# Performance work log

Hardware: AMD Instinct MI355X
Metric: run time of the kernel (lower is better)

Reference implementation:

```python
import jax, jax.numpy as jnp
import numpy as np

B, C, D, H, W = 8, 512, 512, 128, 128


def setup_inputs() -> dict:
    key = jax.random.key(0)
    ks = jax.random.split(key, 6)
    s = 0.02  # small init scale for stable softmax
    return {
        "x": jax.random.normal(ks[0], (B, C, H, W), dtype=jnp.float32),
        "context": jax.random.normal(ks[1], (B, D), dtype=jnp.float32),
        "Wq": jax.random.normal(ks[2], (C, D), dtype=jnp.float32) * s,
        "bq": jnp.ones((C,), dtype=jnp.float32),
        "Wk": jax.random.normal(ks[3], (C, C), dtype=jnp.float32) * s,
        "bk": jnp.zeros((C,), dtype=jnp.float32),
        "Wv": jax.random.normal(ks[4], (C, C), dtype=jnp.float32) * s,
        "bv": jnp.zeros((C,), dtype=jnp.float32),
    }


def reference(x, context, Wq, bq, Wk, bk, Wv, bv):
    # x: (B,C,H,W), context: (B,D)
    scale = x.shape[1] ** (-0.5)
    # q_proj: Linear(D -> C), single query per batch element
    q = context @ Wq.T + bq                      # (B, C)
    # 1x1 convs are channel-mixing GEMMs over the spatial grid
    k = jnp.einsum('bchw,oc->bohw', x, Wk) + bk[None, :, None, None]  # (B,C,H,W)
    v = jnp.einsum('bchw,oc->bohw', x, Wv) + bv[None, :, None, None]  # (B,C,H,W)
    # attention logits over the HW positions (query length == 1)
    logits = jnp.einsum('bc,bchw->bhw', q, k) * scale                 # (B,H,W)
    Bn, Hn, Wn = logits.shape
    attn = jax.nn.softmax(logits.reshape(Bn, Hn * Wn), axis=-1).reshape(Bn, Hn, Wn)
    # attention-pooled value -> channel gate
    gate = jnp.einsum('bhw,bchw->bc', attn, v)                        # (B,C)
    return x * gate[:, :, None, None]
```

## Files before the change

### kernel.cpp

```cpp
#include <hip/hip_runtime.h>
#include <math.h>

#define BB   8
#define CC   512
#define DD   512
#define HW   16384
#define HW4  4096
#define NCHUNK 64


__global__ __launch_bounds__(256) void k_qk2(const float* __restrict__ ctx,
                                             const float* __restrict__ Wq,
                                             const float* __restrict__ bq,
                                             const float* __restrict__ Wk,
                                             float* __restrict__ qk) {
    __shared__ float qs[CC];
    int b    = blockIdx.x >> 1;
    int half = blockIdx.x & 1;
    const float4* cr = (const float4*)(ctx + (size_t)b * DD);
    for (int c = threadIdx.x; c < CC; c += 256) {
        const float4* wr = (const float4*)(Wq + (size_t)c * DD);
        float acc = 0.f;
        #pragma unroll 8
        for (int d = 0; d < DD / 4; ++d) {
            float4 a = cr[d], w = wr[d];
            acc += a.x * w.x + a.y * w.y + a.z * w.z + a.w * w.w;
        }
        qs[c] = acc + bq[c];
    }
    __syncthreads();
    int c = half * 256 + threadIdx.x;
    float acc = 0.f;
    #pragma unroll 8
    for (int o = 0; o < CC; ++o) acc += qs[o] * Wk[(size_t)o * CC + c];
    qk[b * CC + c] = acc;
}

__global__ __launch_bounds__(256) void k_logits_p(const float* __restrict__ x,
                                                  const float* __restrict__ qk,
                                                  float* __restrict__ p,
                                                  float* __restrict__ stats) {
    __shared__ float  qs[CC];
    __shared__ float4 comb[3][64];
    int b     = blockIdx.x >> 6;
    int chunk = blockIdx.x & 63;
    int wave = threadIdx.x >> 6, lane = threadIdx.x & 63;
    int hw4 = chunk * 64 + lane;
    for (int i = threadIdx.x; i < CC; i += 256) qs[i] = qk[b * CC + i];
    __syncthreads();
    const float4* x4 = (const float4*)x;
    size_t base = (size_t)b * CC * HW4 + (size_t)(wave * 128) * HW4 + hw4;
    float ax = 0.f, ay = 0.f, az = 0.f, aw = 0.f;
    #pragma unroll 8
    for (int c = 0; c < 128; ++c) {
        float4 v = x4[base + (size_t)c * HW4];
        float w = qs[wave * 128 + c];
        ax += w * v.x; ay += w * v.y; az += w * v.z; aw += w * v.w;
    }
    if (wave > 0) {
        float4 pp = { ax, ay, az, aw };
        comb[wave - 1][lane] = pp;
    }
    __syncthreads();
    if (wave == 0) {
        #pragma unroll
        for (int w2 = 0; w2 < 3; ++w2) {
            float4 pp = comb[w2][lane];
            ax += pp.x; ay += pp.y; az += pp.z; aw += pp.w;
        }
        const float scale = 0.04419417382415922f;
        ax *= scale; ay *= scale; az *= scale; aw *= scale;
        float m = fmaxf(fmaxf(ax, ay), fmaxf(az, aw));
        #pragma unroll
        for (int off = 32; off; off >>= 1) m = fmaxf(m, __shfl_xor(m, off));
        float4 o;
        o.x = expf(ax - m); o.y = expf(ay - m);
        o.z = expf(az - m); o.w = expf(aw - m);
        float s = o.x + o.y + o.z + o.w;
        #pragma unroll
        for (int off = 32; off; off >>= 1) s += __shfl_xor(s, off);
        ((float4*)p)[(size_t)b * HW4 + hw4] = o;
        if (lane == 0) { stats[blockIdx.x * 2] = m; stats[blockIdx.x * 2 + 1] = s; }
    }
}

__global__ __launch_bounds__(256) void k_pool(const float* __restrict__ x,
                                              const float* __restrict__ p,
                                              const float* __restrict__ stats,
                                              float* __restrict__ pooled) {
    __shared__ float wgt[NCHUNK];
    int bc = blockIdx.x;
    int b  = bc >> 9;
    int tid = threadIdx.x;
    if (tid < 64) {
        float mc = stats[(b * NCHUNK + tid) * 2];
        float sc = stats[(b * NCHUNK + tid) * 2 + 1];
        float m = mc;
        #pragma unroll
        for (int off = 32; off; off >>= 1) m = fmaxf(m, __shfl_xor(m, off));
        float w = expf(mc - m);
        float d = w * sc;
        #pragma unroll
        for (int off = 32; off; off >>= 1) d += __shfl_xor(d, off);
        wgt[tid] = w / d;
    }
    __syncthreads();
    const float4* xr = (const float4*)x + (size_t)bc * HW4;
    const float4* pr = (const float4*)p + (size_t)b  * HW4;
    float acc = 0.f;
    #pragma unroll 8
    for (int i = tid; i < HW4; i += 256) {
        float4 xv = xr[i], pv = pr[i];
        acc += wgt[i >> 6] * (xv.x * pv.x + xv.y * pv.y + xv.z * pv.z + xv.w * pv.w);
    }
    for (int off = 32; off; off >>= 1) acc += __shfl_down(acc, off);
    __shared__ float red[4];
    if ((tid & 63) == 0) red[tid >> 6] = acc;
    __syncthreads();
    if (tid == 0) pooled[bc] = red[0] + red[1] + red[2] + red[3];
}

__global__ __launch_bounds__(256) void k_gate(const float* __restrict__ pooled,
                                              const float* __restrict__ Wv,
                                              const float* __restrict__ bv,
                                              float* __restrict__ gate) {
    int t = blockIdx.x * 256 + threadIdx.x;
    int b = t >> 9, o = t & (CC - 1);
    const float4* pr = (const float4*)(pooled + (size_t)b * CC);
    const float4* wr = (const float4*)(Wv + (size_t)o * CC);
    float acc = 0.f;
    #pragma unroll 8
    for (int i = 0; i < CC / 4; ++i) {
        float4 pv = pr[i], w = wr[i];
        acc += pv.x * w.x + pv.y * w.y + pv.z * w.z + pv.w * w.w;
    }
    gate[t] = acc + bv[o];
}

__global__ __launch_bounds__(256) void k_out(const float* __restrict__ x,
                                             const float* __restrict__ gate,
                                             float* __restrict__ out) {
    int bc = blockIdx.x;
    float g = gate[bc];
    const float4* xr = (const float4*)x   + (size_t)bc * HW4;
    float4*       orow = (float4*)out     + (size_t)bc * HW4;
    #pragma unroll 8
    for (int i = threadIdx.x; i < HW4; i += 256) {
        float4 v = xr[i];
        float4 o = { v.x * g, v.y * g, v.z * g, v.w * g };
        orow[i] = o;
    }
}

extern "C" void kernel_launch(void* const* d_in, const int* in_sizes, int n_in,
                              void* d_out, int out_size, void* d_ws, size_t ws_size,
                              hipStream_t stream) {
    const float* x   = (const float*)d_in[0];
    const float* ctx = (const float*)d_in[1];
    const float* Wq  = (const float*)d_in[2];
    const float* bq  = (const float*)d_in[3];
    const float* Wk  = (const float*)d_in[4];
    const float* Wv  = (const float*)d_in[6];
    const float* bv  = (const float*)d_in[7];
    float* out = (float*)d_out;

    float* ws     = (float*)d_ws;
    float* qk     = ws;
    float* pooled = ws + 4096;
    float* gate   = ws + 8192;
    float* stats  = ws + 12288;
    float* p      = ws + 13312;

    k_qk2     <<<  16, 256, 0, stream>>>(ctx, Wq, bq, Wk, qk);
    k_logits_p<<< 512, 256, 0, stream>>>(x, qk, p, stats);
    k_pool    <<<4096, 256, 0, stream>>>(x, p, stats, pooled);
    k_gate    <<<  16, 256, 0, stream>>>(pooled, Wv, bv, gate);
    k_out     <<<4096, 256, 0, stream>>>(x, gate, out);
}
```

Before: 618.9 us.

## Fuse logits, softmax and pooling into one pass over x with partial sums

Merges the logits/softmax kernel and the pooling kernel so each block loads a tile of x (all channels, 32 positions) into registers once. From those registers it computes the logits, a local softmax and per-channel weighted partial sums. A new combine kernel rescales the 512 per-chunk partials with online-softmax statistics to produce the pooled vector. This removes one full read of x and the p round-trip, at the cost of writing and reading 8×512×512 partials and using more registers per thread.

```diff
diff --git a/kernel.cpp b/kernel.cpp
--- a/kernel.cpp
+++ b/kernel.cpp
@@ -6,7 +6,7 @@
 #define DD   512
 #define HW   16384
 #define HW4  4096
-#define NCHUNK 64
+#define NCH  512
 
 
 __global__ __launch_bounds__(256) void k_qk2(const float* __restrict__ ctx,
@@ -36,88 +36,105 @@
     qk[b * CC + c] = acc;
 }
 
-__global__ __launch_bounds__(256) void k_logits_p(const float* __restrict__ x,
+__global__ __launch_bounds__(512, 4) void k_fused(const float* __restrict__ x,
                                                   const float* __restrict__ qk,
-                                                  float* __restrict__ p,
+                                                  float* __restrict__ part,
                                                   float* __restrict__ stats) {
-    __shared__ float  qs[CC];
-    __shared__ float4 comb[3][64];
-    int b     = blockIdx.x >> 6;
-    int chunk = blockIdx.x & 63;
-    int wave = threadIdx.x >> 6, lane = threadIdx.x & 63;
-    int hw4 = chunk * 64 + lane;
-    for (int i = threadIdx.x; i < CC; i += 256) qs[i] = qk[b * CC + i];
+    __shared__ float qs[CC];
+    __shared__ float4 comb[7][8];
+    __shared__ float4 p4s[8];
+    __shared__ __align__(16) float partLDS[CC];
+    int b   = blockIdx.x >> 9;
+    int cid = blockIdx.x & (NCH - 1);
+    int tid = threadIdx.x;
+    int w = tid >> 6, l = tid & 63;
+    int lg = l >> 3, lp = l & 7;
+    for (int i = tid; i < CC; i += 512) qs[i] = qk[b * CC + i];
     __syncthreads();
     const float4* x4 = (const float4*)x;
-    size_t base = (size_t)b * CC * HW4 + (size_t)(wave * 128) * HW4 + hw4;
-    float ax = 0.f, ay = 0.f, az = 0.f, aw = 0.f;
-    #pragma unroll 8
-    for (int c = 0; c < 128; ++c) {
-        float4 v = x4[base + (size_t)c * HW4];
-        float w = qs[wave * 128 + c];
-        ax += w * v.x; ay += w * v.y; az += w * v.z; aw += w * v.w;
+    size_t base = ((size_t)(b * CC + 64 * w + lg)) * HW4 + cid * 8 + lp;
+    float4 xr[8];
+    #pragma unroll
+    for (int it = 0; it < 8; ++it) xr[it] = x4[base + (size_t)it * 8 * HW4];
+    float4 la = { 0.f, 0.f, 0.f, 0.f };
+    #pragma unroll
+    for (int it = 0; it < 8; ++it) {
+        float qv = qs[64 * w + 8 * it + lg];
+        la.x += qv * xr[it].x; la.y += qv * xr[it].y;
+        la.z += qv * xr[it].z; la.w += qv * xr[it].w;
     }
-    if (wave > 0) {
-        float4 pp = { ax, ay, az, aw };
-        comb[wave - 1][lane] = pp;
+    #pragma unroll
+    for (int st = 8; st <= 32; st <<= 1) {
+        la.x += __shfl_xor(la.x, st); la.y += __shfl_xor(la.y, st);
+        la.z += __shfl_xor(la.z, st); la.w += __shfl_xor(la.w, st);
+    }
+    if (w > 0 && l < 8) comb[w - 1][l] = la;
+    __syncthreads();
+    if (w == 0 && l < 8) {
+        #pragma unroll
+        for (int i = 0; i < 7; ++i) {
+            float4 t = comb[i][l];
+            la.x += t.x; la.y += t.y; la.z += t.z; la.w += t.w;
+        }
+        const float scale = 0.04419417382415922f;
+        la.x *= scale; la.y *= scale; la.z *= scale; la.w *= scale;
+        float m = fmaxf(fmaxf(la.x, la.y), fmaxf(la.z, la.w));
+        m = fmaxf(m, __shfl_xor(m, 1));
+        m = fmaxf(m, __shfl_xor(m, 2));
+        m = fmaxf(m, __shfl_xor(m, 4));
+        float4 p;
+        p.x = expf(la.x - m); p.y = expf(la.y - m);
+        p.z = expf(la.z - m); p.w = expf(la.w - m);
+        float s = p.x + p.y + p.z + p.w;
+        s += __shfl_xor(s, 1); s += __shfl_xor(s, 2); s += __shfl_xor(s, 4);
+        p4s[l] = p;
+        if (l == 0) { stats[blockIdx.x * 2] = m; stats[blockIdx.x * 2 + 1] = s; }
     }
     __syncthreads();
-    if (wave == 0) {
-        #pragma unroll
-        for (int w2 = 0; w2 < 3; ++w2) {
-            float4 pp = comb[w2][lane];
-            ax += pp.x; ay += pp.y; az += pp.z; aw += pp.w;
-        }
-        const float scale = 0.04419417382415922f;
-        ax *= scale; ay *= scale; az *= scale; aw *= scale;
-        float m = fmaxf(fmaxf(ax, ay), fmaxf(az, aw));
-        #pragma unroll
-        for (int off = 32; off; off >>= 1) m = fmaxf(m, __shfl_xor(m, off));
-        float4 o;
-        o.x = expf(ax - m); o.y = expf(ay - m);
-        o.z = expf(az - m); o.w = expf(aw - m);
-        float s = o.x + o.y + o.z + o.w;
-        #pragma unroll
-        for (int off = 32; off; off >>= 1) s += __shfl_xor(s, off);
-        ((float4*)p)[(size_t)b * HW4 + hw4] = o;
-        if (lane == 0) { stats[blockIdx.x * 2] = m; stats[blockIdx.x * 2 + 1] = s; }
+    float4 pw = p4s[lp];
+    #pragma unroll
+    for (int it = 0; it < 8; ++it) {
+        float r = pw.x * xr[it].x + pw.y * xr[it].y + pw.z * xr[it].z + pw.w * xr[it].w;
+        r += __shfl_xor(r, 1); r += __shfl_xor(r, 2); r += __shfl_xor(r, 4);
+        if (lp == 0) partLDS[64 * w + 8 * it + lg] = r;
     }
+    __syncthreads();
+    if (tid < CC / 4)
+        ((float4*)(part + (size_t)blockIdx.x * CC))[tid] = ((float4*)partLDS)[tid];
 }
 
-__global__ __launch_bounds__(256) void k_pool(const float* __restrict__ x,
-                                              const float* __restrict__ p,
-                                              const float* __restrict__ stats,
-                                              float* __restrict__ pooled) {
-    __shared__ float wgt[NCHUNK];
-    int bc = blockIdx.x;
-    int b  = bc >> 9;
+__global__ __launch_bounds__(256) void k_combine(const float* __restrict__ part,
+                                                 const float* __restrict__ stats,
+                                                 float* __restrict__ pooled) {
+    __shared__ float wgt[NCH];
+    __shared__ float redm[4], reds[4];
+    int b = blockIdx.x >> 1, half = blockIdx.x & 1;
     int tid = threadIdx.x;
-    if (tid < 64) {
-        float mc = stats[(b * NCHUNK + tid) * 2];
-        float sc = stats[(b * NCHUNK + tid) * 2 + 1];
-        float m = mc;
-        #pragma unroll
-        for (int off = 32; off; off >>= 1) m = fmaxf(m, __shfl_xor(m, off));
-        float w = expf(mc - m);
-        float d = w * sc;
-        #pragma unroll
-        for (int off = 32; off; off >>= 1) d += __shfl_xor(d, off);
-        wgt[tid] = w / d;
-    }
+    float m1 = stats[((size_t)b * NCH + tid) * 2];
+    float s1 = stats[((size_t)b * NCH + tid) * 2 + 1];
+    float m2 = stats[((size_t)b * NCH + tid + 256) * 2];
+    float s2 = stats[((size_t)b * NCH + tid + 256) * 2 + 1];
+    float m = fmaxf(m1, m2);
+    #pragma unroll
+    for (int off = 32; off; off >>= 1) m = fmaxf(m, __shfl_xor(m, off));
+    if ((tid & 63) == 0) redm[tid >> 6] = m;
     __syncthreads();
-    const float4* xr = (const float4*)x + (size_t)bc * HW4;
-    const float4* pr = (const float4*)p + (size_t)b  * HW4;
+    m = fmaxf(fmaxf(redm[0], redm[1]), fmaxf(redm[2], redm[3]));
+    float w1 = expf(m1 - m), w2 = expf(m2 - m);
+    float d = w1 * s1 + w2 * s2;
+    #pragma unroll
+    for (int off = 32; off; off >>= 1) d += __shfl_xor(d, off);
+    if ((tid & 63) == 0) reds[tid >> 6] = d;
+    __syncthreads();
+    float inv = 1.f / (reds[0] + reds[1] + reds[2] + reds[3]);
+    wgt[tid] = w1 * inv; wgt[tid + 256] = w2 * inv;
+    __syncthreads();
+    int c = half * 256 + tid;
     float acc = 0.f;
     #pragma unroll 8
-    for (int i = tid; i < HW4; i += 256) {
-        float4 xv = xr[i], pv = pr[i];
-        acc += wgt[i >> 6] * (xv.x * pv.x + xv.y * pv.y + xv.z * pv.z + xv.w * pv.w);
-    }
-    for (int off = 32; off; off >>= 1) acc += __shfl_down(acc, off);
-    __shared__ float red[4];
-    if ((tid & 63) == 0) red[tid >> 6] = acc;
-    __syncthreads();
-    if (tid == 0) pooled[bc] = red[0] + red[1] + red[2] + red[3];
+    for (int ch = 0; ch < NCH; ++ch)
+        acc += wgt[ch] * part[((size_t)b * NCH + ch) * CC + c];
+    pooled[b * CC + c] = acc;
 }
 
 __global__ __launch_bounds__(256) void k_gate(const float* __restrict__ pooled,
@@ -169,11 +186,11 @@
     float* pooled = ws + 4096;
     float* gate   = ws + 8192;
     float* stats  = ws + 12288;
-    float* p      = ws + 13312;
+    float* part   = ws + 20480;
 
-    k_qk2     <<<  16, 256, 0, stream>>>(ctx, Wq, bq, Wk, qk);
-    k_logits_p<<< 512, 256, 0, stream>>>(x, qk, p, stats);
-    k_pool    <<<4096, 256, 0, stream>>>(x, p, stats, pooled);
-    k_gate    <<<  16, 256, 0, stream>>>(pooled, Wv, bv, gate);
-    k_out     <<<4096, 256, 0, stream>>>(x, gate, out);
+    k_qk2    <<<  16, 256, 0, stream>>>(ctx, Wq, bq, Wk, qk);
+    k_fused  <<<4096, 512, 0, stream>>>(x, qk, part, stats);
+    k_combine<<<  16, 256, 0, stream>>>(part, stats, pooled);
+    k_gate   <<<  16, 256, 0, stream>>>(pooled, Wv, bv, gate);
+    k_out    <<<4096, 256, 0, stream>>>(x, gate, out);
 }
```

New measurement: 622.6 us. About the same (+0.6%).
